# Optimization experiments

Hardware: AMD Instinct MI355X
Metric: run time of the kernel (lower is better)

The kernel has to match this reference:

```python
import jax, jax.numpy as jnp
import numpy as np

N = 10000      # nodes
E = 320000     # edges (avg degree 32)
C = 256        # feature dim (input_dim == output_dim)
L = 3          # num_layers
D = 20         # KAF dictionary size
BOUNDARY = 4.0 # KAF dictionary boundary


def setup_inputs() -> dict:
    key = jax.random.key(0)
    ks = jax.random.split(key, 7)
    x = jax.random.normal(ks[0], (N, C), jnp.float32)
    edge_index = jax.random.randint(ks[1], (2, E), 0, N, jnp.int32)
    edge_attr = jax.random.normal(ks[2], (E, 2), jnp.float32)
    # per-layer stacked parameters (all layers have identical shapes)
    node_w = jax.random.normal(ks[3], (L, C, C), jnp.float32) / jnp.sqrt(jnp.float32(C))
    edge_w = jax.random.normal(ks[4], (L, 2, C), jnp.float32) / jnp.sqrt(jnp.float32(2))
    neigh_w = jax.random.normal(ks[5], (L, C, C), jnp.float32) / jnp.sqrt(jnp.float32(C))
    bias = jnp.zeros((L, C), jnp.float32)
    alpha = jax.random.normal(ks[6], (L, C, D), jnp.float32) * 0.3
    return dict(x=x, edge_index=edge_index, edge_attr=edge_attr,
                node_w=node_w, edge_w=edge_w, neigh_w=neigh_w, bias=bias, alpha=alpha)


def _kaf(s, alpha_l):
    # Kernel Activation Function (Scardapane et al.): per-channel Gaussian mixture
    dict_pts = jnp.linspace(-BOUNDARY, BOUNDARY, D, dtype=s.dtype)  # [D]
    interval = 2.0 * BOUNDARY / (D - 1)
    gamma = 0.5 / (2.0 * interval) ** 2
    K = jnp.exp(-gamma * jnp.square(s[..., None] - dict_pts))  # [N, C, D]
    return jnp.einsum('ncd,cd->nc', K, alpha_l)


def reference(x, edge_index, edge_attr, node_w, edge_w, neigh_w, bias, alpha):
    src, dst = edge_index[0], edge_index[1]
    # mean-aggregation normalizer (computed once; graph is fixed across layers)
    cnt = jax.ops.segment_sum(jnp.ones((E,), x.dtype), dst, num_segments=N)
    inv_cnt = jnp.where(cnt > 0, 1.0 / jnp.maximum(cnt, 1.0), 0.0)  # [N]
    h = x
    for l in range(L):
        # message: edge_attr @ W_e + x_j @ W_n  -> [E, C]
        msg = edge_attr @ edge_w[l] + h[src] @ neigh_w[l]
        # mean aggregate to destination nodes
        aggr = jax.ops.segment_sum(msg, dst, num_segments=N) * inv_cnt[:, None]
        # update: KAF(aggr + x @ W + b)
        h = _kaf(aggr + h @ node_w[l] + bias[l], alpha[l])
    return h
```

## Files before the change

### kernel.cpp

```cpp
#include <hip/hip_runtime.h>
#include <hip/hip_bf16.h>

#define N_NODES 10000
#define N_EDGES 320000
#define CDIM    256
#define B_PRE   80
#define EPB     (N_EDGES / B_PRE)
#define SLK     130
#define SA      86

typedef __attribute__((ext_vector_type(8))) _Float16 half8;
typedef __attribute__((ext_vector_type(4))) _Float16 half4;
typedef __attribute__((ext_vector_type(4))) float floatx4;

#define OFF_RS    0
#define OFF_INVC  40960
#define OFF_S2    81920
#define OFF_COLV  163840
#define OFF_WCAT  806912
#define OFF_HN    1593344
#define OFF_HX    6713344
#define OFF_PERC  OFF_HN
#define OFF_BASE  (OFF_HN + 1600000)
#define OFF_EA2   OFF_HX
#define OFF_CTOT  (OFF_HX + 2560000)

__global__ __launch_bounds__(256) void k_prep(const float4* __restrict__ x, half4* __restrict__ hB,
                                              const float* __restrict__ neigh_w, const float* __restrict__ node_w,
                                              _Float16* __restrict__ wcatT) {
  __shared__ float t[32][33];
  const int b = blockIdx.x;
  if (b < 2500) {
    int i = b * 256 + threadIdx.x;
    float4 v = x[i];
    half4 h; h.x = (_Float16)v.x; h.y = (_Float16)v.y; h.z = (_Float16)v.z; h.w = (_Float16)v.w;
    hB[i] = h;
    return;
  }
  const int bb = b - 2500;
  const int k0 = (bb & 7) * 32;
  const int n0 = ((bb >> 3) & 15) * 32;
  const int l  = bb >> 7;
  const int tx = threadIdx.x & 31;
  const int ty = threadIdx.x >> 5;
  const float* src = (n0 < 256) ? neigh_w : node_w;
  const int nb = (n0 < 256) ? n0 : (n0 - 256);
#pragma unroll
  for (int p = 0; p < 4; ++p) {
    int k = k0 + ty + p * 8;
    t[ty + p * 8][tx] = src[l * 65536 + k * 256 + (nb + tx)];
  }
  __syncthreads();
#pragma unroll
  for (int p = 0; p < 4; ++p) {
    int n = n0 + ty + p * 8;
    wcatT[(size_t)l * 131072 + n * 256 + (k0 + tx)] = (_Float16)t[tx][ty + p * 8];
  }
}

__global__ __launch_bounds__(1024) void k_count(const int* __restrict__ ei,
                                                unsigned short* __restrict__ percnt) {
  __shared__ int hist[N_NODES];
  const int t = threadIdx.x, b = blockIdx.x;
  for (int n = t; n < N_NODES; n += 1024) hist[n] = 0;
  __syncthreads();
  const int e0 = b * EPB;
  for (int e = e0 + t; e < e0 + EPB; e += 1024)
    atomicAdd(&hist[ei[N_EDGES + e]], 1);
  __syncthreads();
  for (int n = t; n < N_NODES; n += 1024)
    percnt[b * N_NODES + n] = (unsigned short)hist[n];
}

__global__ __launch_bounds__(256) void k_base(const unsigned short* __restrict__ percnt,
                                              int* __restrict__ prefix, int* __restrict__ cnttot) {
  int n = blockIdx.x * 256 + threadIdx.x;
  if (n >= N_NODES) return;
  int s = 0;
  for (int b = 0; b < B_PRE; ++b) {
    prefix[b * N_NODES + n] = s;
    s += (int)percnt[b * N_NODES + n];
  }
  cnttot[n] = s;
}

__global__ __launch_bounds__(1024) void k_scan(const int* __restrict__ cnttot,
                                               int* __restrict__ rs, float* __restrict__ invc) {
  __shared__ int lds[1024];
  const int t = threadIdx.x;
  const int base = t * 10;
  int loc[10];
  int sum = 0;
#pragma unroll
  for (int i = 0; i < 10; ++i) {
    int idx = base + i;
    int v = (idx < N_NODES) ? cnttot[idx] : 0;
    loc[i] = v; sum += v;
  }
  lds[t] = sum; __syncthreads();
  for (int off = 1; off < 1024; off <<= 1) {
    int v = 0;
    if (t >= off) v = lds[t - off];
    __syncthreads();
    if (t >= off) lds[t] += v;
    __syncthreads();
  }
  int ex = lds[t] - sum;
#pragma unroll
  for (int i = 0; i < 10; ++i) {
    int idx = base + i;
    if (idx < N_NODES) {
      rs[idx] = ex; ex += loc[i];
      invc[idx] = (loc[i] > 0) ? (1.0f / (float)loc[i]) : 0.0f;
    }
  }
  if (t == 1023) rs[N_NODES] = lds[1023];
}

__global__ __launch_bounds__(1024) void k_scat(const int* __restrict__ ei, const float* __restrict__ ea,
                                               const int* __restrict__ prefix, const int* __restrict__ rs,
                                               unsigned short* __restrict__ colv, float2* __restrict__ ea2) {
  __shared__ int cur[N_NODES];
  const int t = threadIdx.x, b = blockIdx.x;
  for (int n = t; n < N_NODES; n += 1024)
    cur[n] = rs[n] + prefix[b * N_NODES + n];
  __syncthreads();
  const int e0 = b * EPB;
  for (int e = e0 + t; e < e0 + EPB; e += 1024) {
    int d = ei[N_EDGES + e];
    int src = ei[e];
    float2 a = ((const float2*)ea)[e];
    int pos = atomicAdd(&cur[d], 1);
    colv[pos] = (unsigned short)src;
    ea2[pos] = a;
  }
}

__global__ __launch_bounds__(256) void k_s2(const int* __restrict__ rs, const float2* __restrict__ ea2,
                                            float* __restrict__ s2) {
  int n = blockIdx.x * 256 + threadIdx.x;
  if (n >= N_NODES) return;
  int beg = rs[n], end = rs[n + 1];
  float sx = 0.f, sy = 0.f;
  for (int p = beg; p < end; ++p) { float2 a = ea2[p]; sx += a.x; sy += a.y; }
  s2[2 * n] = sx; s2[2 * n + 1] = sy;
}

__global__ __launch_bounds__(256) void k_gemm(const _Float16* __restrict__ A,
                                              const _Float16* __restrict__ BT,
                                              _Float16* __restrict__ hn,
                                              _Float16* __restrict__ hx) {
  __shared__ _Float16 As[64 * SLK];
  __shared__ _Float16 Bs[64 * SLK];
  const int tid = threadIdx.x;
  const int wv = tid >> 6;
  const int lane = tid & 63;
  const int m0 = blockIdx.x * 64;
  const int n0 = blockIdx.y * 64;
  const int wy = wv >> 1, wx = wv & 1;

  floatx4 acc[2][2];
#pragma unroll
  for (int i = 0; i < 2; ++i)
#pragma unroll
    for (int j = 0; j < 2; ++j) acc[i][j] = (floatx4){0.f, 0.f, 0.f, 0.f};

  const int mrow = 32 * wy + (lane & 15);
  const int nrow = 32 * wx + (lane & 15);
  const int q8 = (lane >> 4) * 8;

#pragma unroll
  for (int kt = 0; kt < 2; ++kt) {
    half8 av[4], bv[4];
#pragma unroll
    for (int c = 0; c < 4; ++c) {
      int ch = tid + 256 * c;
      int row = ch >> 4;
      int off = (ch & 15) * 8;
      int arow = m0 + row; if (arow >= N_NODES) arow = N_NODES - 1;
      av[c] = *(const half8*)(A + (size_t)arow * 256 + kt * 128 + off);
      bv[c] = *(const half8*)(BT + (size_t)(n0 + row) * 256 + kt * 128 + off);
    }
    __syncthreads();
#pragma unroll
    for (int c = 0; c < 4; ++c) {
      int ch = tid + 256 * c;
      int row = ch >> 4;
      int off = (ch & 15) * 8;
      *(half8*)&As[row * SLK + off] = av[c];
      *(half8*)&Bs[row * SLK + off] = bv[c];
    }
    __syncthreads();
#pragma unroll
    for (int ks = 0; ks < 4; ++ks) {
      const int kb = ks * 32 + q8;
      half8 af0 = *(const half8*)&As[mrow * SLK + kb];
      half8 af1 = *(const half8*)&As[(mrow + 16) * SLK + kb];
      half8 bf0 = *(const half8*)&Bs[nrow * SLK + kb];
      half8 bf1 = *(const half8*)&Bs[(nrow + 16) * SLK + kb];
      acc[0][0] = __builtin_amdgcn_mfma_f32_16x16x32_f16(af0, bf0, acc[0][0], 0, 0, 0);
      acc[0][1] = __builtin_amdgcn_mfma_f32_16x16x32_f16(af0, bf1, acc[0][1], 0, 0, 0);
      acc[1][0] = __builtin_amdgcn_mfma_f32_16x16x32_f16(af1, bf0, acc[1][0], 0, 0, 0);
      acc[1][1] = __builtin_amdgcn_mfma_f32_16x16x32_f16(af1, bf1, acc[1][1], 0, 0, 0);
    }
  }

  const int colb = n0 + 32 * wx + (lane & 15);
  const int rowb = m0 + 32 * wy + 4 * (lane >> 4);
#pragma unroll
  for (int i = 0; i < 2; ++i) {
#pragma unroll
    for (int j = 0; j < 2; ++j) {
      const int cn = colb + 16 * j;
#pragma unroll
      for (int r = 0; r < 4; ++r) {
        const int rw = rowb + 16 * i + r;
        if (rw < N_NODES) {
          float v = acc[i][j][r];
          if (cn < 256) hn[rw * 256 + cn] = (_Float16)v;
          else          hx[rw * 256 + (cn - 256)] = (_Float16)v;
        }
      }
    }
  }
}

__global__ __launch_bounds__(256) void k_update(const int* __restrict__ rs, const unsigned short* __restrict__ colv,
                                                const float* __restrict__ invc, const float* __restrict__ s2,
                                                const _Float16* __restrict__ hn, const _Float16* __restrict__ hx,
                                                const float* __restrict__ ew,
                                                const float* __restrict__ bias,
                                                const float* __restrict__ alpha,
                                                _Float16* __restrict__ hmid, float* __restrict__ fout,
                                                int final_layer) {
  __shared__ float alds[64 * SA];
#pragma unroll
  for (int i = 0; i < 20; ++i) {
    int s = threadIdx.x + 256 * i;
    int c = s / 20, j = s - 20 * c;
    alds[(c >> 2) * SA + 4 * j + (c & 3)] = alpha[s];
  }
  __syncthreads();

  const int wv   = threadIdx.x >> 6;
  const int lane = threadIdx.x & 63;
  const int hf   = lane >> 5;
  const int l5   = lane & 31;
  const int n = blockIdx.x * 4 + wv;
  int beg = rs[n], end = rs[n + 1];
  beg = max(0, min(beg, N_EDGES));
  end = max(beg, min(end, N_EDGES));
  const int co = l5 * 8;

  half8 acc0 = (half8)(_Float16)0.f, acc1 = (half8)(_Float16)0.f;
  half8 acc2 = (half8)(_Float16)0.f, acc3 = (half8)(_Float16)0.f;
  for (int base = beg; base < end; base += 64) {
    const int cnt = min(64, end - base);
    int myIdx = 0;
    if (base + lane < end) myIdx = (int)colv[base + lane];
    int j = 0;
    for (; j + 8 <= cnt; j += 8) {
      int s0 = __shfl(myIdx, j + hf);
      int s1 = __shfl(myIdx, j + 2 + hf);
      int s2i = __shfl(myIdx, j + 4 + hf);
      int s3 = __shfl(myIdx, j + 6 + hf);
      half8 v0 = *(const half8*)(hn + (size_t)s0 * 256 + co);
      half8 v1 = *(const half8*)(hn + (size_t)s1 * 256 + co);
      half8 v2 = *(const half8*)(hn + (size_t)s2i * 256 + co);
      half8 v3 = *(const half8*)(hn + (size_t)s3 * 256 + co);
      acc0 += v0; acc1 += v1; acc2 += v2; acc3 += v3;
    }
    for (; j + 2 <= cnt; j += 2) {
      int s0 = __shfl(myIdx, j + hf);
      acc0 += *(const half8*)(hn + (size_t)s0 * 256 + co);
    }
    if (j < cnt) {
      int s0 = __shfl(myIdx, j);
      if (hf == 0)
        acc0 += *(const half8*)(hn + (size_t)s0 * 256 + co);
    }
  }
  acc0 = (acc0 + acc2) + (acc1 + acc3);
  union { half8 h; unsigned int u[4]; } me, ot;
  me.h = acc0;
#pragma unroll
  for (int r = 0; r < 4; ++r) ot.u[r] = (unsigned int)__shfl_xor((int)me.u[r], 32);
  acc0 = me.h + ot.h;

  const int c0 = l5 * 8 + hf * 4;
  float a0, a1, a2, a3;
  if (hf) { a0 = (float)acc0[4]; a1 = (float)acc0[5]; a2 = (float)acc0[6]; a3 = (float)acc0[7]; }
  else    { a0 = (float)acc0[0]; a1 = (float)acc0[1]; a2 = (float)acc0[2]; a3 = (float)acc0[3]; }

  const int q = c0 >> 2;
  const float ic = invc[n];
  const float t0 = s2[2 * n], t1 = s2[2 * n + 1];
  const half4  hv = ((const half4*)hx)[n * 64 + q];
  const float4 e0 = ((const float4*)ew)[q];
  const float4 e1 = ((const float4*)ew)[64 + q];
  const float4 bi = ((const float4*)bias)[q];
  float s[4];
  s[0] = (a0 + t0 * e0.x + t1 * e1.x) * ic + (float)hv.x + bi.x;
  s[1] = (a1 + t0 * e0.y + t1 * e1.y) * ic + (float)hv.y + bi.y;
  s[2] = (a2 + t0 * e0.z + t1 * e1.z) * ic + (float)hv.z + bi.z;
  s[3] = (a3 + t0 * e0.w + t1 * e1.w) * ic + (float)hv.w + bi.w;

  const float G = -0.705078125f;
  const float dp = 8.0f / 19.0f;
  const float* ar = &alds[q * SA];
  float o0 = 0.f, o1 = 0.f, o2 = 0.f, o3 = 0.f;
#pragma unroll
  for (int j = 0; j < 20; ++j) {
    float2 a01 = *(const float2*)(ar + 4 * j);
    float2 a23 = *(const float2*)(ar + 4 * j + 2);
    const float p = -4.0f + dp * (float)j;
    float x0 = s[0] - p, x1 = s[1] - p, x2 = s[2] - p, x3 = s[3] - p;
    o0 += a01.x * __expf(G * x0 * x0);
    o1 += a01.y * __expf(G * x1 * x1);
    o2 += a23.x * __expf(G * x2 * x2);
    o3 += a23.y * __expf(G * x3 * x3);
  }
  if (final_layer) {
    float4 w; w.x = o0; w.y = o1; w.z = o2; w.w = o3;
    ((float4*)fout)[n * 64 + q] = w;
  } else {
    half4 w; w.x = (_Float16)o0; w.y = (_Float16)o1; w.z = (_Float16)o2; w.w = (_Float16)o3;
    ((half4*)hmid)[n * 64 + q] = w;
  }
}

extern "C" void kernel_launch(void* const* d_in, const int* in_sizes, int n_in,
                              void* d_out, int out_size, void* d_ws, size_t ws_size,
                              hipStream_t stream) {
  const float* x       = (const float*)d_in[0];
  const int*   ei      = (const int*)d_in[1];
  const float* ea      = (const float*)d_in[2];
  const float* node_w  = (const float*)d_in[3];
  const float* edge_w  = (const float*)d_in[4];
  const float* neigh_w = (const float*)d_in[5];
  const float* bias    = (const float*)d_in[6];
  const float* alpha   = (const float*)d_in[7];

  char* w = (char*)d_ws;
  int*            rs     = (int*)(w + OFF_RS);
  float*          invc   = (float*)(w + OFF_INVC);
  float*          s2     = (float*)(w + OFF_S2);
  unsigned short* colv   = (unsigned short*)(w + OFF_COLV);
  _Float16*       wcatT  = (_Float16*)(w + OFF_WCAT);
  _Float16*       hn     = (_Float16*)(w + OFF_HN);
  _Float16*       hx     = (_Float16*)(w + OFF_HX);
  unsigned short* percnt = (unsigned short*)(w + OFF_PERC);
  int*            prefix = (int*)(w + OFF_BASE);
  float2*         ea2    = (float2*)(w + OFF_EA2);
  int*            cnttot = (int*)(w + OFF_CTOT);
  float*          fout   = (float*)d_out;
  _Float16*       hB     = (_Float16*)d_out;

  k_prep<<<2884, 256, 0, stream>>>((const float4*)x, (half4*)hB, neigh_w, node_w, wcatT);
  k_count<<<B_PRE, 1024, 0, stream>>>(ei, percnt);
  k_base<<<40, 256, 0, stream>>>(percnt, prefix, cnttot);
  k_scan<<<1, 1024, 0, stream>>>(cnttot, rs, invc);
  k_scat<<<B_PRE, 1024, 0, stream>>>(ei, ea, prefix, rs, colv, ea2);
  k_s2<<<40, 256, 0, stream>>>(rs, ea2, s2);

  for (int l = 0; l < 3; ++l) {
    k_gemm<<<dim3(157, 8, 1), 256, 0, stream>>>(hB, wcatT + l * 131072, hn, hx);
    k_update<<<2500, 256, 0, stream>>>(rs, colv, invc, s2, hn, hx,
                                       edge_w + l * 512, bias + l * 256, alpha + l * 5120,
                                       hB, fout, (l == 2) ? 1 : 0);
  }
}
```

Baseline: 230.0 us.

## Merge preprocessing kernels and enlarge update blocks to cut launch count

Folds the fp16 conversion, weight transpose and per-chunk edge counting into one launch, and fuses the per-node base prefix with the global scan using a last-block-done atomic counter. This removes two kernel launches and their serialization gaps. It also raises k_update to 1024-thread blocks covering 16 nodes each, so the alpha table is staged into LDS once per 16 nodes instead of once per 4. The risks are that the counting blocks now run with 256 threads instead of 1024, and the large block size may reduce occupancy.

```diff
diff --git a/kernel.cpp b/kernel.cpp
--- a/kernel.cpp
+++ b/kernel.cpp
@@ -24,11 +24,13 @@
 #define OFF_BASE  (OFF_HN + 1600000)
 #define OFF_EA2   OFF_HX
 #define OFF_CTOT  (OFF_HX + 2560000)
-
-__global__ __launch_bounds__(256) void k_prep(const float4* __restrict__ x, half4* __restrict__ hB,
-                                              const float* __restrict__ neigh_w, const float* __restrict__ node_w,
-                                              _Float16* __restrict__ wcatT) {
-  __shared__ float t[32][33];
+#define OFF_DONE  (OFF_HX + 2600000)
+
+__global__ __launch_bounds__(256) void k_phase1(const float4* __restrict__ x, half4* __restrict__ hB,
+                                                const float* __restrict__ neigh_w, const float* __restrict__ node_w,
+                                                _Float16* __restrict__ wcatT,
+                                                const int* __restrict__ ei, unsigned short* __restrict__ percnt,
+                                                int* __restrict__ done) {
   const int b = blockIdx.x;
   if (b < 2500) {
     int i = b * 256 + threadIdx.x;
@@ -37,57 +39,66 @@
     hB[i] = h;
     return;
   }
-  const int bb = b - 2500;
-  const int k0 = (bb & 7) * 32;
-  const int n0 = ((bb >> 3) & 15) * 32;
-  const int l  = bb >> 7;
-  const int tx = threadIdx.x & 31;
-  const int ty = threadIdx.x >> 5;
-  const float* src = (n0 < 256) ? neigh_w : node_w;
-  const int nb = (n0 < 256) ? n0 : (n0 - 256);
-#pragma unroll
-  for (int p = 0; p < 4; ++p) {
-    int k = k0 + ty + p * 8;
-    t[ty + p * 8][tx] = src[l * 65536 + k * 256 + (nb + tx)];
-  }
-  __syncthreads();
-#pragma unroll
-  for (int p = 0; p < 4; ++p) {
-    int n = n0 + ty + p * 8;
-    wcatT[(size_t)l * 131072 + n * 256 + (k0 + tx)] = (_Float16)t[tx][ty + p * 8];
-  }
-}
-
-__global__ __launch_bounds__(1024) void k_count(const int* __restrict__ ei,
-                                                unsigned short* __restrict__ percnt) {
+  if (b < 2884) {
+    __shared__ float t[32][33];
+    const int bb = b - 2500;
+    const int k0 = (bb & 7) * 32;
+    const int n0 = ((bb >> 3) & 15) * 32;
+    const int l  = bb >> 7;
+    const int tx = threadIdx.x & 31;
+    const int ty = threadIdx.x >> 5;
+    const float* src = (n0 < 256) ? neigh_w : node_w;
+    const int nb = (n0 < 256) ? n0 : (n0 - 256);
+#pragma unroll
+    for (int p = 0; p < 4; ++p) {
+      int k = k0 + ty + p * 8;
+      t[ty + p * 8][tx] = src[l * 65536 + k * 256 + (nb + tx)];
+    }
+    __syncthreads();
+#pragma unroll
+    for (int p = 0; p < 4; ++p) {
+      int n = n0 + ty + p * 8;
+      wcatT[(size_t)l * 131072 + n * 256 + (k0 + tx)] = (_Float16)t[tx][ty + p * 8];
+    }
+    return;
+  }
   __shared__ int hist[N_NODES];
-  const int t = threadIdx.x, b = blockIdx.x;
-  for (int n = t; n < N_NODES; n += 1024) hist[n] = 0;
-  __syncthreads();
-  const int e0 = b * EPB;
-  for (int e = e0 + t; e < e0 + EPB; e += 1024)
+  const int cb = b - 2884;
+  const int t = threadIdx.x;
+  if (b == 2884 && t == 0) *done = 0;
+  for (int n = t; n < N_NODES; n += 256) hist[n] = 0;
+  __syncthreads();
+  const int e0 = cb * EPB;
+  for (int e = e0 + t; e < e0 + EPB; e += 256)
     atomicAdd(&hist[ei[N_EDGES + e]], 1);
   __syncthreads();
-  for (int n = t; n < N_NODES; n += 1024)
-    percnt[b * N_NODES + n] = (unsigned short)hist[n];
-}
-
-__global__ __launch_bounds__(256) void k_base(const unsigned short* __restrict__ percnt,
-                                              int* __restrict__ prefix, int* __restrict__ cnttot) {
-  int n = blockIdx.x * 256 + threadIdx.x;
-  if (n >= N_NODES) return;
-  int s = 0;
-  for (int b = 0; b < B_PRE; ++b) {
-    prefix[b * N_NODES + n] = s;
-    s += (int)percnt[b * N_NODES + n];
-  }
-  cnttot[n] = s;
-}
-
-__global__ __launch_bounds__(1024) void k_scan(const int* __restrict__ cnttot,
-                                               int* __restrict__ rs, float* __restrict__ invc) {
+  for (int n = t; n < N_NODES; n += 256)
+    percnt[cb * N_NODES + n] = (unsigned short)hist[n];
+}
+
+__global__ __launch_bounds__(1024) void k_basescan(const unsigned short* __restrict__ percnt,
+                                                   int* __restrict__ prefix, int* __restrict__ cnttot,
+                                                   int* __restrict__ done,
+                                                   int* __restrict__ rs, float* __restrict__ invc) {
   __shared__ int lds[1024];
+  __shared__ int amLast;
   const int t = threadIdx.x;
+  const int n = blockIdx.x * 1024 + t;
+  if (n < N_NODES) {
+    int s = 0;
+    for (int b = 0; b < B_PRE; ++b) {
+      prefix[b * N_NODES + n] = s;
+      s += (int)percnt[b * N_NODES + n];
+    }
+    cnttot[n] = s;
+  }
+  __threadfence();
+  __syncthreads();
+  if (t == 0) amLast = (atomicAdd(done, 1) == gridDim.x - 1) ? 1 : 0;
+  __syncthreads();
+  if (!amLast) return;
+  __threadfence();
+
   const int base = t * 10;
   int loc[10];
   int sum = 0;
@@ -225,18 +236,18 @@
   }
 }
 
-__global__ __launch_bounds__(256) void k_update(const int* __restrict__ rs, const unsigned short* __restrict__ colv,
-                                                const float* __restrict__ invc, const float* __restrict__ s2,
-                                                const _Float16* __restrict__ hn, const _Float16* __restrict__ hx,
-                                                const float* __restrict__ ew,
-                                                const float* __restrict__ bias,
-                                                const float* __restrict__ alpha,
-                                                _Float16* __restrict__ hmid, float* __restrict__ fout,
-                                                int final_layer) {
+__global__ __launch_bounds__(1024) void k_update(const int* __restrict__ rs, const unsigned short* __restrict__ colv,
+                                                 const float* __restrict__ invc, const float* __restrict__ s2,
+                                                 const _Float16* __restrict__ hn, const _Float16* __restrict__ hx,
+                                                 const float* __restrict__ ew,
+                                                 const float* __restrict__ bias,
+                                                 const float* __restrict__ alpha,
+                                                 _Float16* __restrict__ hmid, float* __restrict__ fout,
+                                                 int final_layer) {
   __shared__ float alds[64 * SA];
 #pragma unroll
-  for (int i = 0; i < 20; ++i) {
-    int s = threadIdx.x + 256 * i;
+  for (int i = 0; i < 5; ++i) {
+    int s = threadIdx.x + 1024 * i;
     int c = s / 20, j = s - 20 * c;
     alds[(c >> 2) * SA + 4 * j + (c & 3)] = alpha[s];
   }
@@ -246,7 +257,7 @@
   const int lane = threadIdx.x & 63;
   const int hf   = lane >> 5;
   const int l5   = lane & 31;
-  const int n = blockIdx.x * 4 + wv;
+  const int n = blockIdx.x * 16 + wv;
   int beg = rs[n], end = rs[n + 1];
   beg = max(0, min(beg, N_EDGES));
   end = max(beg, min(end, N_EDGES));
@@ -353,19 +364,19 @@
   int*            prefix = (int*)(w + OFF_BASE);
   float2*         ea2    = (float2*)(w + OFF_EA2);
   int*            cnttot = (int*)(w + OFF_CTOT);
+  int*            done   = (int*)(w + OFF_DONE);
   float*          fout   = (float*)d_out;
   _Float16*       hB     = (_Float16*)d_out;
 
-  k_prep<<<2884, 256, 0, stream>>>((const float4*)x, (half4*)hB, neigh_w, node_w, wcatT);
-  k_count<<<B_PRE, 1024, 0, stream>>>(ei, percnt);
-  k_base<<<40, 256, 0, stream>>>(percnt, prefix, cnttot);
-  k_scan<<<1, 1024, 0, stream>>>(cnttot, rs, invc);
+  k_phase1<<<2964, 256, 0, stream>>>((const float4*)x, (half4*)hB, neigh_w, node_w, wcatT,
+                                     ei, percnt, done);
+  k_basescan<<<10, 1024, 0, stream>>>(percnt, prefix, cnttot, done, rs, invc);
   k_scat<<<B_PRE, 1024, 0, stream>>>(ei, ea, prefix, rs, colv, ea2);
   k_s2<<<40, 256, 0, stream>>>(rs, ea2, s2);
 
   for (int l = 0; l < 3; ++l) {
     k_gemm<<<dim3(157, 8, 1), 256, 0, stream>>>(hB, wcatT + l * 131072, hn, hx);
-    k_update<<<2500, 256, 0, stream>>>(rs, colv, invc, s2, hn, hx,
+    k_update<<<625, 1024, 0, stream>>>(rs, colv, invc, s2, hn, hx,
                                        edge_w + l * 512, bias + l * 256, alpha + l * 5120,
                                        hB, fout, (l == 2) ? 1 : 0);
   }
```

Result: slower. 264.8 us (+15.1%).
